# Kernel optimization log

Measured on AMD Instinct MI355X. Metric: run time of the kernel, lower is better.

The kernel has to match this reference:

```python
import jax, jax.numpy as jnp
import numpy as np

N_NODES = 50000
NUM_FEAT = 2000
HEADS = 8
HID = 8
NUM_CLASSES = 30
NUM_EDGES = 1_600_000
NEG_SLOPE = 0.2


def _segment_softmax(scores, seg, num_segments):
    # scores: [E, H], seg: [E] destination node ids
    m = jax.ops.segment_max(scores, seg, num_segments=num_segments)
    m = jnp.where(jnp.isfinite(m), m, 0.0)  # guard empty segments
    e = jnp.exp(scores - m[seg])
    s = jax.ops.segment_sum(e, seg, num_segments=num_segments)
    return e / (s[seg] + 1e-16)


def _gat_layer(x, src, dst, w, att_src, att_dst, bias, concat):
    # PyG GATConv (eval mode: dropout disabled). x: [N, F_in]
    n = x.shape[0]
    h_, c_ = att_src.shape
    h = (x @ w).reshape(n, h_, c_)                      # [N, H, C]
    a_src = (h * att_src[None]).sum(-1)                 # [N, H]
    a_dst = (h * att_dst[None]).sum(-1)                 # [N, H]
    alpha = jax.nn.leaky_relu(a_src[src] + a_dst[dst], NEG_SLOPE)  # [E, H]
    alpha = _segment_softmax(alpha, dst, n)             # per-dest softmax
    msg = h[src] * alpha[:, :, None]                    # [E, H, C]
    out = jax.ops.segment_sum(msg, dst, num_segments=n) # [N, H, C]
    out = out.reshape(n, h_ * c_) if concat else out.mean(axis=1)
    return out + bias, alpha


def _add_self_loops(edge_index, n):
    loops = jnp.arange(n, dtype=edge_index.dtype)
    src = jnp.concatenate([edge_index[0], loops])
    dst = jnp.concatenate([edge_index[1], loops])
    return src, dst


def setup_inputs() -> dict:
    key = jax.random.key(0)
    ks = jax.random.split(key, 12)
    x = jax.random.normal(ks[0], (N_NODES, NUM_FEAT), jnp.float32)
    edge_index = jax.random.randint(ks[1], (2, NUM_EDGES), 0, N_NODES, jnp.int32)
    d1 = HEADS * HID
    w_res = jax.random.normal(ks[2], (NUM_FEAT, d1), jnp.float32) / np.sqrt(NUM_FEAT)
    b_res = jnp.zeros((d1,), jnp.float32)
    w1 = jax.random.normal(ks[3], (NUM_FEAT, d1), jnp.float32) / np.sqrt(NUM_FEAT)
    att_src1 = jax.random.normal(ks[4], (HEADS, HID), jnp.float32) * 0.1
    att_dst1 = jax.random.normal(ks[5], (HEADS, HID), jnp.float32) * 0.1
    b1 = jnp.zeros((d1,), jnp.float32)
    w2 = jax.random.normal(ks[6], (d1, NUM_CLASSES), jnp.float32) / np.sqrt(d1)
    att_src2 = jax.random.normal(ks[7], (1, NUM_CLASSES), jnp.float32) * 0.1
    att_dst2 = jax.random.normal(ks[8], (1, NUM_CLASSES), jnp.float32) * 0.1
    b2 = jnp.zeros((NUM_CLASSES,), jnp.float32)
    return {"x": x, "edge_index": edge_index, "w_res": w_res, "b_res": b_res,
            "w1": w1, "att_src1": att_src1, "att_dst1": att_dst1, "b1": b1,
            "w2": w2, "att_src2": att_src2, "att_dst2": att_dst2, "b2": b2}


def reference(x, edge_index, w_res, b_res, w1, att_src1, att_dst1, b1,
              w2, att_src2, att_dst2, b2):
    n = x.shape[0]
    src, dst = _add_self_loops(edge_index, n)
    res = x @ w_res + b_res                                   # residual branch
    h1, alpha1 = _gat_layer(x, src, dst, w1, att_src1, att_dst1, b1, concat=True)
    x1 = jax.nn.elu(h1 + res)                                 # dropout = identity (eval)
    h2, alpha2 = _gat_layer(x1, src, dst, w2, att_src2, att_dst2, b2, concat=False)
    x2 = jax.nn.elu(h2)
    return jax.nn.log_softmax(x2, axis=1), alpha1, alpha2
```

## Files before the change

kernel.cpp:

```cpp
#include <hip/hip_runtime.h>
#include <hip/hip_bf16.h>

#define N_NODES 50000
#define NUM_FEAT 2000
#define HEADS 8
#define HID 8
#define NUM_CLASSES 30
#define NUM_EDGES 1600000
#define E_TOTAL (NUM_EDGES + N_NODES)
#define E8 (E_TOTAL * 8)
#define KT32 64
#define KT64 32
#define ROWCAP 128
#define GEMM_BLOCKS ((N_NODES + 63) / 64)
#define FILL_BLOCKS ((E_TOTAL + 255) / 256)
#define LOG2E 1.44269504f
#define SENT N_NODES
#define NEG_BIG -1.0e30f

typedef __attribute__((ext_vector_type(8))) short short8;
typedef __attribute__((ext_vector_type(4))) float f32x4;

typedef __attribute__((address_space(1))) const unsigned int gu32;
typedef __attribute__((address_space(3))) unsigned int lu32;

__device__ __forceinline__ void gload_lds16(const void* g, void* l) {
  __builtin_amdgcn_global_load_lds((gu32*)g, (lu32*)l, 16, 0, 0);
}

__device__ __forceinline__ ushort f2bf(float f) {
  __hip_bfloat16 b = __float2bfloat16(f);
  return *reinterpret_cast<ushort*>(&b);
}

__device__ __forceinline__ float bf2f(ushort u) {
  unsigned int x = ((unsigned int)u) << 16;
  union { unsigned int i; float f; } c; c.i = x;
  return c.f;
}

__device__ __forceinline__ float lexp2(float sc) {
  return exp2f(fmaxf(sc, 0.2f * sc));
}

__device__ __forceinline__ short8 cvt8(float4 a, float4 b) {
  union { short8 v; ushort u[8]; } p;
  p.u[0] = f2bf(a.x); p.u[1] = f2bf(a.y); p.u[2] = f2bf(a.z); p.u[3] = f2bf(a.w);
  p.u[4] = f2bf(b.x); p.u[5] = f2bf(b.y); p.u[6] = f2bf(b.z); p.u[7] = f2bf(b.w);
  return p.v;
}

__global__ __launch_bounds__(256) void k_init(int* __restrict__ esrc,
    const float* __restrict__ Wres, const float* __restrict__ W1,
    ushort* __restrict__ Bp, int* __restrict__ cursor) {
  int i = blockIdx.x * 256 + threadIdx.x;
  if (i < N_NODES * ROWCAP / 4)
    *(int4*)&esrc[i * 4] = make_int4(SENT, SENT, SENT, SENT);
  if (i < N_NODES / 4)
    *(int4*)&cursor[i * 4] = make_int4(0, 0, 0, 0);
  if (i < KT32 * 4 * 128) {
    int col = i & 127;
    int kbase = (i >> 7) * 8;
    const float* W = (col < 64) ? Wres : W1;
    int c = col & 63;
    union { short8 v; ushort u[8]; } p;
#pragma unroll
    for (int j = 0; j < 8; ++j) {
      int k = kbase + j;
      p.u[j] = f2bf(k < NUM_FEAT ? W[(size_t)k * 64 + c] : 0.f);
    }
    *(short8*)&Bp[(size_t)i * 8] = p.v;
  }
}

__global__ __launch_bounds__(256) void k_gemm_fill(const float* __restrict__ X,
    const ushort* __restrict__ Bp, const float* __restrict__ brs,
    const float* __restrict__ b1, float* __restrict__ Hres,
    ushort* __restrict__ Hatt, const int* __restrict__ ei,
    int* __restrict__ cursor, int* __restrict__ esrc) {
  __shared__ ushort ldsB[2][8192];
  if (blockIdx.x >= GEMM_BLOCKS) {
    int e = (blockIdx.x - GEMM_BLOCKS) * 256 + threadIdx.x;
    if (e < E_TOTAL) {
      int s, d;
      if (e < NUM_EDGES) { s = ei[e]; d = ei[NUM_EDGES + e]; }
      else { s = d = e - NUM_EDGES; }
      int pos = atomicAdd(&cursor[d], 1);
      esrc[(unsigned)(d * ROWCAP + pos)] = s;
    }
    return;
  }
  const int tid = threadIdx.x;
  const int lane = tid & 63, wid = tid >> 6;
  const int lg = lane >> 4, lr = lane & 15;
  const int m0 = blockIdx.x * 64;

  int rowg = m0 + wid * 16 + lr;
  rowg = rowg < N_NODES ? rowg : N_NODES - 1;
  const float* axp = X + (size_t)rowg * NUM_FEAT + lg * 8;

  f32x4 acc[8] = {};
  float4 a[4], na[4];
  const float4 fz = make_float4(0.f, 0.f, 0.f, 0.f);

  auto loadA = [&](int t, float4* r) {
#pragma unroll
    for (int s = 0; s < 2; ++s) {
      int k0 = t * 64 + s * 32 + lg * 8;
      if (k0 < NUM_FEAT) {
        r[2 * s]     = *(const float4*)(axp + t * 64 + s * 32);
        r[2 * s + 1] = *(const float4*)(axp + t * 64 + s * 32 + 4);
      } else { r[2 * s] = fz; r[2 * s + 1] = fz; }
    }
  };
  auto dmaB = [&](int t, int buf) {
#pragma unroll
    for (int q = 0; q < 4; ++q) {
      const ushort* g = Bp + ((size_t)t * 1024 + q * 256 + wid * 64 + lane) * 8;
      gload_lds16(g, &ldsB[buf][(size_t)(q * 256 + wid * 64) * 8]);
    }
  };
  auto mfmaStep = [&](int cur, const float4* av) {
#pragma unroll
    for (int s = 0; s < 2; ++s) {
      short8 fb[8];
#pragma unroll
      for (int n = 0; n < 8; ++n)
        fb[n] = *(const short8*)&ldsB[cur][(size_t)(s * 512 + lg * 128 + n * 16 + lr) * 8];
      short8 fa = cvt8(av[2 * s], av[2 * s + 1]);
#pragma unroll
      for (int n = 0; n < 8; ++n)
        acc[n] = __builtin_amdgcn_mfma_f32_16x16x32_bf16(fa, fb[n], acc[n], 0, 0, 0);
    }
  };

  dmaB(0, 0);
  __builtin_amdgcn_sched_barrier(0);
  loadA(0, a);
  asm volatile("s_waitcnt vmcnt(4)" ::: "memory");
  __builtin_amdgcn_s_barrier();
  __builtin_amdgcn_sched_barrier(0);

  for (int t = 0; t < KT64 - 1; ++t) {
    const int cur = t & 1, nxt = cur ^ 1;
    dmaB(t + 1, nxt);
    __builtin_amdgcn_sched_barrier(0);
    loadA(t + 1, na);
    mfmaStep(cur, a);
    asm volatile("s_waitcnt vmcnt(4)" ::: "memory");
    __builtin_amdgcn_s_barrier();
    __builtin_amdgcn_sched_barrier(0);
#pragma unroll
    for (int q = 0; q < 4; ++q) a[q] = na[q];
  }
  mfmaStep((KT64 - 1) & 1, a);

#pragma unroll
  for (int n = 0; n < 8; ++n) {
    int col = n * 16 + lr;
    if (col < 64) {
      float badd = brs[col] + b1[col];
#pragma unroll
      for (int i = 0; i < 4; ++i) {
        int row = m0 + wid * 16 + lg * 4 + i;
        if (row < N_NODES) Hres[(size_t)row * 64 + col] = acc[n][i] + badd;
      }
    } else {
#pragma unroll
      for (int i = 0; i < 4; ++i) {
        int row = m0 + wid * 16 + lg * 4 + i;
        if (row < N_NODES) Hatt[(size_t)row * 64 + (col - 64)] = f2bf(acc[n][i]);
      }
    }
  }
}

__global__ void k_attn1(ushort* __restrict__ Hatt,
                        const float* __restrict__ att_src,
                        const float* __restrict__ att_dst,
                        float* __restrict__ a_src, float2* __restrict__ dinv1) {
  int i = blockIdx.x * 256 + threadIdx.x;
  if (i < N_NODES * HEADS) {
    int h = i & 7;
    const ushort* hp = &Hatt[(size_t)(i >> 3) * 64 + h * 8];
    float s = 0.f, d = 0.f;
#pragma unroll
    for (int c = 0; c < 8; ++c) {
      float v = bf2f(hp[c]);
      s = fmaf(v, att_src[h * 8 + c], s);
      d = fmaf(v, att_dst[h * 8 + c], d);
    }
    a_src[i] = s * LOG2E;
    dinv1[i] = make_float2(d * LOG2E, 0.f);
  }
  if (i < 64) Hatt[(size_t)SENT * 64 + i] = 0;
  if (i >= 64 && i < 72) a_src[SENT * 8 + (i - 64)] = NEG_BIG;
}

__global__ __launch_bounds__(256) void k_layer1f(const int* __restrict__ esrc,
    const int* __restrict__ cursor,
    const float* __restrict__ Hres, const ushort* __restrict__ Hatt,
    const float* __restrict__ a_src, float2* __restrict__ dinv1,
    const float* __restrict__ w2, const float* __restrict__ att_src2,
    const float* __restrict__ att_dst2, ushort* __restrict__ h2b,
    float* __restrict__ a_src2, float2* __restrict__ dinv2) {
  __shared__ float w2s[64 * 30];
  __shared__ float xs[4][64];
  for (int i = threadIdx.x; i < 64 * 30; i += 256) w2s[i] = w2[i];
  if (blockIdx.x == 0) {
    if (threadIdx.x < 32) h2b[(unsigned)(SENT * 32 + threadIdx.x)] = 0;
    if (threadIdx.x == 32) a_src2[SENT] = NEG_BIG;
  }
  __syncthreads();
  int wave = threadIdx.x >> 6, lane = threadIdx.x & 63;
  int n = blockIdx.x * 4 + wave;
  if (n >= N_NODES) return;
  int hd = lane >> 3;
  float adn = dinv1[(unsigned)(n * 8 + hd)].x;
  int start = n * ROWCAP, end = start + ((cursor[n] + 7) & ~7);
  float denom = 0.f, msg = 0.f;
  for (int p = start; p < end; p += 8) {
    int4 v0 = *(const int4*)&esrc[p];
    int4 v1 = *(const int4*)&esrc[p + 4];
    int s8[8] = {v0.x, v0.y, v0.z, v0.w, v1.x, v1.y, v1.z, v1.w};
    float av[8];
    ushort hu[8];
#pragma unroll
    for (int i = 0; i < 8; ++i) {
      av[i] = a_src[(unsigned)(s8[i] * 8 + hd)];
      hu[i] = Hatt[(unsigned)(s8[i] * 64 + lane)];
    }
#pragma unroll
    for (int i = 0; i < 8; ++i) {
      float ev = lexp2(av[i] + adn);
      denom += ev;
      msg = fmaf(ev, bf2f(hu[i]), msg);
    }
  }
  float invd = 1.f / (denom + 1e-16f);
  float x1v = msg * invd + Hres[(unsigned)(n * 64 + lane)];
  x1v = x1v > 0.f ? x1v : __expf(x1v) - 1.f;
  if ((lane & 7) == 0) dinv1[(unsigned)(n * 8 + hd)].y = invd;

  xs[wave][lane] = x1v;
  float acc2 = 0.f;
  if (lane < 30) {
#pragma unroll 8
    for (int k = 0; k < 64; ++k) acc2 = fmaf(xs[wave][k], w2s[k * 30 + lane], acc2);
  }
  float as = (lane < 30) ? acc2 * att_src2[lane] : 0.f;
  float ad = (lane < 30) ? acc2 * att_dst2[lane] : 0.f;
  for (int off = 1; off < 64; off <<= 1) {
    as += __shfl_xor(as, off);
    ad += __shfl_xor(ad, off);
  }
  if (lane == 0) { a_src2[n] = as * LOG2E; dinv2[n] = make_float2(ad * LOG2E, 0.f); }
  if (lane < 32) h2b[(unsigned)(n * 32 + lane)] = (lane < 30) ? f2bf(acc2) : (ushort)0;
}

__global__ __launch_bounds__(256) void k_layer2(const int* __restrict__ esrc,
    const int* __restrict__ cursor,
    const ushort* __restrict__ h2b, const float* __restrict__ a_src2,
    float2* __restrict__ dinv2, const float* __restrict__ b2,
    float* __restrict__ out0) {
  int wave = threadIdx.x >> 6, lane = threadIdx.x & 63;
  int n = blockIdx.x * 4 + wave;
  if (n >= N_NODES) return;
  float adn = dinv2[n].x;
  int start = n * ROWCAP, end = start + ((cursor[n] + 7) & ~7);
  int half = lane >> 5, cls = lane & 31;
  float denom = 0.f, msg = 0.f;
  for (int p = start; p < end; p += 4) {
    int s0 = esrc[p + half];
    int s1 = esrc[p + 2 + half];
    float as0 = a_src2[(unsigned)s0], as1 = a_src2[(unsigned)s1];
    ushort hv0 = h2b[(unsigned)(s0 * 32 + cls)];
    ushort hv1 = h2b[(unsigned)(s1 * 32 + cls)];
    float ev0 = lexp2(as0 + adn);
    denom += ev0;
    msg = fmaf(ev0, bf2f(hv0), msg);
    float ev1 = lexp2(as1 + adn);
    denom += ev1;
    msg = fmaf(ev1, bf2f(hv1), msg);
  }
  denom += __shfl_xor(denom, 32);
  msg   += __shfl_xor(msg, 32);
  float invd = 1.f / (denom + 1e-16f);
  bool act = lane < 30;
  float o = act ? msg * invd + b2[lane] : 0.f;
  float x2 = o > 0.f ? o : __expf(o) - 1.f;
  float mv = act ? x2 : -1e30f;
  for (int off = 1; off < 64; off <<= 1) mv = fmaxf(mv, __shfl_xor(mv, off));
  float ex = act ? __expf(x2 - mv) : 0.f;
  for (int off = 1; off < 64; off <<= 1) ex += __shfl_xor(ex, off);
  if (act) out0[(size_t)n * 30 + lane] = x2 - mv - __logf(ex);
  if (lane == 0) dinv2[n].y = invd;
}

__global__ __launch_bounds__(256) void k_alpha(const int* __restrict__ ei,
    const float* __restrict__ a_src1, const float2* __restrict__ dinv1,
    const float* __restrict__ a_src2, const float2* __restrict__ dinv2,
    float* __restrict__ alpha1, float* __restrict__ alpha2) {
  int i = blockIdx.x * 256 + threadIdx.x;
  if (i >= E8) return;
  {
    int e = i >> 3, h = i & 7;
    int s, d;
    if (e < NUM_EDGES) { s = ei[e]; d = ei[NUM_EDGES + e]; }
    else { s = d = e - NUM_EDGES; }
    float2 di = dinv1[(unsigned)(d * 8 + h)];
    alpha1[i] = lexp2(a_src1[(unsigned)(s * 8 + h)] + di.x) * di.y;
  }
  if (i < E_TOTAL) {
    int s, d;
    if (i < NUM_EDGES) { s = ei[i]; d = ei[NUM_EDGES + i]; }
    else { s = d = i - NUM_EDGES; }
    float2 dj = dinv2[(unsigned)d];
    alpha2[i] = lexp2(a_src2[(unsigned)s] + dj.x) * dj.y;
  }
}

extern "C" void kernel_launch(void* const* d_in, const int* in_sizes, int n_in,
                              void* d_out, int out_size, void* d_ws, size_t ws_size,
                              hipStream_t stream) {
  const float* x        = (const float*)d_in[0];
  const int*   ei       = (const int*)d_in[1];
  const float* w_res    = (const float*)d_in[2];
  const float* b_res    = (const float*)d_in[3];
  const float* w1       = (const float*)d_in[4];
  const float* att_src1 = (const float*)d_in[5];
  const float* att_dst1 = (const float*)d_in[6];
  const float* b1       = (const float*)d_in[7];
  const float* w2       = (const float*)d_in[8];
  const float* att_src2 = (const float*)d_in[9];
  const float* att_dst2 = (const float*)d_in[10];
  const float* b2       = (const float*)d_in[11];

  float* ws = (float*)d_ws;
  float* Hres    = ws;
  float* a_src1  = Hres + (size_t)N_NODES * 64;
  float2* dinv1  = (float2*)(a_src1 + (size_t)(N_NODES + 1) * 8);
  float* a_src2  = (float*)(dinv1 + (size_t)N_NODES * 8);
  float2* dinv2  = (float2*)(a_src2 + N_NODES + 1);
  ushort* Hatt   = (ushort*)(dinv2 + N_NODES);
  ushort* h2b    = Hatt + (size_t)(N_NODES + 1) * 64;
  ushort* Bp     = h2b + (size_t)(N_NODES + 1) * 32 + 32;
  int*   cursor  = (int*)(Bp + (size_t)KT32 * 4096 + 64);

  float* out0   = (float*)d_out;
  float* alpha1 = out0 + (size_t)N_NODES * 30;
  float* alpha2 = alpha1 + (size_t)E8;
  int*   esrc   = (int*)alpha1;

  k_init<<<(N_NODES * ROWCAP / 4 + 255) / 256, 256, 0, stream>>>(esrc, w_res, w1,
                                                                 Bp, cursor);
  k_gemm_fill<<<GEMM_BLOCKS + FILL_BLOCKS, 256, 0, stream>>>(x, Bp, b_res, b1,
                                                             Hres, Hatt, ei,
                                                             cursor, esrc);
  k_attn1<<<(N_NODES * HEADS + 255) / 256, 256, 0, stream>>>(Hatt, att_src1,
                                                             att_dst1, a_src1,
                                                             dinv1);
  k_layer1f<<<(N_NODES + 3) / 4, 256, 0, stream>>>(esrc, cursor, Hres, Hatt,
                                                   a_src1, dinv1, w2, att_src2,
                                                   att_dst2, h2b, a_src2, dinv2);
  k_layer2<<<(N_NODES + 3) / 4, 256, 0, stream>>>(esrc, cursor, h2b, a_src2,
                                                  dinv2, b2, out0);
  k_alpha<<<(E8 + 255) / 256, 256, 0, stream>>>(ei, a_src1, dinv1, a_src2, dinv2,
                                                alpha1, alpha2);
}
```

Measured before the change: 374.8 us.

## Store adjacency as 16-bit indices in workspace and overlap alpha1 with layer 2

Neighbor source ids are now kept as ushort in a dedicated workspace buffer instead of int32 aliased over the alpha1 output. This halves the bytes spent initializing and reading the padded adjacency. Because alpha1 no longer shares storage with the adjacency, its computation is folded into the layer-2 aggregation launch as extra blocks, which lets it overlap with layer 2. Alpha2 stays in its own small kernel. The change relies on node ids fitting in 16 bits, which holds for 50000 nodes plus the sentinel.

```diff
diff --git a/kernel.cpp b/kernel.cpp
--- a/kernel.cpp
+++ b/kernel.cpp
@@ -14,11 +14,14 @@
 #define ROWCAP 128
 #define GEMM_BLOCKS ((N_NODES + 63) / 64)
 #define FILL_BLOCKS ((E_TOTAL + 255) / 256)
+#define L2_BLOCKS ((N_NODES + 3) / 4)
+#define A1_BLOCKS ((E8 + 255) / 256)
 #define LOG2E 1.44269504f
 #define SENT N_NODES
 #define NEG_BIG -1.0e30f
 
 typedef __attribute__((ext_vector_type(8))) short short8;
+typedef __attribute__((ext_vector_type(8))) unsigned short ushort8;
 typedef __attribute__((ext_vector_type(4))) float f32x4;
 
 typedef __attribute__((address_space(1))) const unsigned int gu32;
@@ -50,12 +53,13 @@
   return p.v;
 }
 
-__global__ __launch_bounds__(256) void k_init(int* __restrict__ esrc,
+__global__ __launch_bounds__(256) void k_init(ushort* __restrict__ esrc,
     const float* __restrict__ Wres, const float* __restrict__ W1,
     ushort* __restrict__ Bp, int* __restrict__ cursor) {
   int i = blockIdx.x * 256 + threadIdx.x;
-  if (i < N_NODES * ROWCAP / 4)
-    *(int4*)&esrc[i * 4] = make_int4(SENT, SENT, SENT, SENT);
+  const unsigned rep = (unsigned)SENT | ((unsigned)SENT << 16);
+  if (i < N_NODES * ROWCAP / 8)
+    ((uint4*)esrc)[i] = make_uint4(rep, rep, rep, rep);
   if (i < N_NODES / 4)
     *(int4*)&cursor[i * 4] = make_int4(0, 0, 0, 0);
   if (i < KT32 * 4 * 128) {
@@ -77,7 +81,7 @@
     const ushort* __restrict__ Bp, const float* __restrict__ brs,
     const float* __restrict__ b1, float* __restrict__ Hres,
     ushort* __restrict__ Hatt, const int* __restrict__ ei,
-    int* __restrict__ cursor, int* __restrict__ esrc) {
+    int* __restrict__ cursor, ushort* __restrict__ esrc) {
   __shared__ ushort ldsB[2][8192];
   if (blockIdx.x >= GEMM_BLOCKS) {
     int e = (blockIdx.x - GEMM_BLOCKS) * 256 + threadIdx.x;
@@ -86,7 +90,7 @@
       if (e < NUM_EDGES) { s = ei[e]; d = ei[NUM_EDGES + e]; }
       else { s = d = e - NUM_EDGES; }
       int pos = atomicAdd(&cursor[d], 1);
-      esrc[(unsigned)(d * ROWCAP + pos)] = s;
+      esrc[(unsigned)(d * ROWCAP + pos)] = (ushort)s;
     }
     return;
   }
@@ -197,7 +201,7 @@
   if (i >= 64 && i < 72) a_src[SENT * 8 + (i - 64)] = NEG_BIG;
 }
 
-__global__ __launch_bounds__(256) void k_layer1f(const int* __restrict__ esrc,
+__global__ __launch_bounds__(256) void k_layer1f(const ushort* __restrict__ esrc,
     const int* __restrict__ cursor,
     const float* __restrict__ Hres, const ushort* __restrict__ Hatt,
     const float* __restrict__ a_src, float2* __restrict__ dinv1,
@@ -220,15 +224,14 @@
   int start = n * ROWCAP, end = start + ((cursor[n] + 7) & ~7);
   float denom = 0.f, msg = 0.f;
   for (int p = start; p < end; p += 8) {
-    int4 v0 = *(const int4*)&esrc[p];
-    int4 v1 = *(const int4*)&esrc[p + 4];
-    int s8[8] = {v0.x, v0.y, v0.z, v0.w, v1.x, v1.y, v1.z, v1.w};
+    ushort8 v = *(const ushort8*)&esrc[p];
     float av[8];
     ushort hu[8];
 #pragma unroll
     for (int i = 0; i < 8; ++i) {
-      av[i] = a_src[(unsigned)(s8[i] * 8 + hd)];
-      hu[i] = Hatt[(unsigned)(s8[i] * 64 + lane)];
+      unsigned s = v[i];
+      av[i] = a_src[s * 8 + hd];
+      hu[i] = Hatt[s * 64 + lane];
     }
 #pragma unroll
     for (int i = 0; i < 8; ++i) {
@@ -258,11 +261,25 @@
   if (lane < 32) h2b[(unsigned)(n * 32 + lane)] = (lane < 30) ? f2bf(acc2) : (ushort)0;
 }
 
-__global__ __launch_bounds__(256) void k_layer2(const int* __restrict__ esrc,
+__global__ __launch_bounds__(256) void k_l2a1(const ushort* __restrict__ esrc,
     const int* __restrict__ cursor,
     const ushort* __restrict__ h2b, const float* __restrict__ a_src2,
     float2* __restrict__ dinv2, const float* __restrict__ b2,
-    float* __restrict__ out0) {
+    float* __restrict__ out0, const int* __restrict__ ei,
+    const float* __restrict__ a_src1, const float2* __restrict__ dinv1,
+    float* __restrict__ alpha1) {
+  if (blockIdx.x >= L2_BLOCKS) {
+    int i = (blockIdx.x - L2_BLOCKS) * 256 + threadIdx.x;
+    if (i < E8) {
+      int e = i >> 3, h = i & 7;
+      int s, d;
+      if (e < NUM_EDGES) { s = ei[e]; d = ei[NUM_EDGES + e]; }
+      else { s = d = e - NUM_EDGES; }
+      float2 di = dinv1[(unsigned)(d * 8 + h)];
+      alpha1[i] = lexp2(a_src1[(unsigned)(s * 8 + h)] + di.x) * di.y;
+    }
+    return;
+  }
   int wave = threadIdx.x >> 6, lane = threadIdx.x & 63;
   int n = blockIdx.x * 4 + wave;
   if (n >= N_NODES) return;
@@ -271,11 +288,11 @@
   int half = lane >> 5, cls = lane & 31;
   float denom = 0.f, msg = 0.f;
   for (int p = start; p < end; p += 4) {
-    int s0 = esrc[p + half];
-    int s1 = esrc[p + 2 + half];
-    float as0 = a_src2[(unsigned)s0], as1 = a_src2[(unsigned)s1];
-    ushort hv0 = h2b[(unsigned)(s0 * 32 + cls)];
-    ushort hv1 = h2b[(unsigned)(s1 * 32 + cls)];
+    unsigned s0 = esrc[p + half];
+    unsigned s1 = esrc[p + 2 + half];
+    float as0 = a_src2[s0], as1 = a_src2[s1];
+    ushort hv0 = h2b[s0 * 32 + cls];
+    ushort hv1 = h2b[s1 * 32 + cls];
     float ev0 = lexp2(as0 + adn);
     denom += ev0;
     msg = fmaf(ev0, bf2f(hv0), msg);
@@ -297,27 +314,16 @@
   if (lane == 0) dinv2[n].y = invd;
 }
 
-__global__ __launch_bounds__(256) void k_alpha(const int* __restrict__ ei,
-    const float* __restrict__ a_src1, const float2* __restrict__ dinv1,
+__global__ __launch_bounds__(256) void k_alpha2(const int* __restrict__ ei,
     const float* __restrict__ a_src2, const float2* __restrict__ dinv2,
-    float* __restrict__ alpha1, float* __restrict__ alpha2) {
+    float* __restrict__ alpha2) {
   int i = blockIdx.x * 256 + threadIdx.x;
-  if (i >= E8) return;
-  {
-    int e = i >> 3, h = i & 7;
-    int s, d;
-    if (e < NUM_EDGES) { s = ei[e]; d = ei[NUM_EDGES + e]; }
-    else { s = d = e - NUM_EDGES; }
-    float2 di = dinv1[(unsigned)(d * 8 + h)];
-    alpha1[i] = lexp2(a_src1[(unsigned)(s * 8 + h)] + di.x) * di.y;
-  }
-  if (i < E_TOTAL) {
-    int s, d;
-    if (i < NUM_EDGES) { s = ei[i]; d = ei[NUM_EDGES + i]; }
-    else { s = d = i - NUM_EDGES; }
-    float2 dj = dinv2[(unsigned)d];
-    alpha2[i] = lexp2(a_src2[(unsigned)s] + dj.x) * dj.y;
-  }
+  if (i >= E_TOTAL) return;
+  int s, d;
+  if (i < NUM_EDGES) { s = ei[i]; d = ei[NUM_EDGES + i]; }
+  else { s = d = i - NUM_EDGES; }
+  float2 dj = dinv2[(unsigned)d];
+  alpha2[i] = lexp2(a_src2[(unsigned)s] + dj.x) * dj.y;
 }
 
 extern "C" void kernel_launch(void* const* d_in, const int* in_sizes, int n_in,
@@ -338,7 +344,8 @@
 
   float* ws = (float*)d_ws;
   float* Hres    = ws;
-  float* a_src1  = Hres + (size_t)N_NODES * 64;
+  ushort* esrc   = (ushort*)(Hres + (size_t)N_NODES * 64);
+  float* a_src1  = (float*)(esrc + (size_t)N_NODES * ROWCAP);
   float2* dinv1  = (float2*)(a_src1 + (size_t)(N_NODES + 1) * 8);
   float* a_src2  = (float*)(dinv1 + (size_t)N_NODES * 8);
   float2* dinv2  = (float2*)(a_src2 + N_NODES + 1);
@@ -350,9 +357,8 @@
   float* out0   = (float*)d_out;
   float* alpha1 = out0 + (size_t)N_NODES * 30;
   float* alpha2 = alpha1 + (size_t)E8;
-  int*   esrc   = (int*)alpha1;
-
-  k_init<<<(N_NODES * ROWCAP / 4 + 255) / 256, 256, 0, stream>>>(esrc, w_res, w1,
+
+  k_init<<<(N_NODES * ROWCAP / 8 + 255) / 256, 256, 0, stream>>>(esrc, w_res, w1,
                                                                  Bp, cursor);
   k_gemm_fill<<<GEMM_BLOCKS + FILL_BLOCKS, 256, 0, stream>>>(x, Bp, b_res, b1,
                                                              Hres, Hatt, ei,
@@ -363,8 +369,8 @@
   k_layer1f<<<(N_NODES + 3) / 4, 256, 0, stream>>>(esrc, cursor, Hres, Hatt,
                                                    a_src1, dinv1, w2, att_src2,
                                                    att_dst2, h2b, a_src2, dinv2);
-  k_layer2<<<(N_NODES + 3) / 4, 256, 0, stream>>>(esrc, cursor, h2b, a_src2,
-                                                  dinv2, b2, out0);
-  k_alpha<<<(E8 + 255) / 256, 256, 0, stream>>>(ei, a_src1, dinv1, a_src2, dinv2,
-                                                alpha1, alpha2);
-}
+  k_l2a1<<<L2_BLOCKS + A1_BLOCKS, 256, 0, stream>>>(esrc, cursor, h2b, a_src2,
+                                                    dinv2, b2, out0, ei,
+                                                    a_src1, dinv1, alpha1);
+  k_alpha2<<<(E_TOTAL + 255) / 256, 256, 0, stream>>>(ei, a_src2, dinv2, alpha2);
+}
```

Result: faster. 365.5 us (-2.5%).
